# Kernel optimization log

Measured on AMD Instinct MI355X. Metric: run time of the kernel, lower is better.

The kernel has to match this reference:

```python
import jax, jax.numpy as jnp
import numpy as np

NEG_INF = -9.0e15  # matches torch's -9000000000000000.0 mask value
ALPHA = 0.2        # LeakyReLU negative slope


def setup_inputs() -> dict:
    key = jax.random.key(0)
    k1, k2, k3, k4 = jax.random.split(key, 4)
    N, F_in, F_out = 8192, 128, 128
    x = jax.random.normal(k1, (N, F_in), dtype=jnp.float32)
    adj = jax.random.randint(k2, (N, N), 0, 2, dtype=jnp.int32)
    W = jax.random.normal(k3, (F_in, F_out), dtype=jnp.float32) * (1.0 / np.sqrt(F_in))
    a = jax.random.normal(k4, (2 * F_out, 1), dtype=jnp.float32) * (1.0 / np.sqrt(2 * F_out))
    return {"x": x, "adj": adj, "W": W, "a": a}


def reference(x, adj, W, a):
    # h = W(input): [N, F_out]
    h = x @ W
    F_out = h.shape[1]
    # a([h_i || h_j]) = h_i . a[:F] + h_j . a[F:]  -- identical math to the
    # original NxNx2F concat, without materializing it.
    a_src = a[:F_out, 0]   # coefficients on the row (i) node
    a_dst = a[F_out:, 0]   # coefficients on the column (j) node
    s_src = h @ a_src      # [N]
    s_dst = h @ a_dst      # [N]
    e = jax.nn.leaky_relu(s_src[:, None] + s_dst[None, :], negative_slope=ALPHA)  # [N, N]
    e = jnp.where(adj > 0, e, jnp.float32(NEG_INF))
    attention = jax.nn.softmax(e, axis=1)
    # dropout omitted (identity at eval) for a deterministic baseline
    h_prime = attention @ h  # [N, F_out]
    return h_prime
```

## Files before the change

kernel.cpp:

```cpp
#include <hip/hip_runtime.h>

#define N 8192
#define F 128
#define ALPHA 0.2f

typedef __attribute__((ext_vector_type(8))) short short8;
typedef __attribute__((ext_vector_type(4))) float f32x4;
typedef unsigned short u16;

__device__ __forceinline__ u16 f2bf(float f) {
    unsigned int u = __float_as_uint(f);
    u += 0x7fff + ((u >> 16) & 1);
    return (u16)(u >> 16);
}
__device__ __forceinline__ float bf2f(u16 b) {
    return __uint_as_float(((unsigned int)b) << 16);
}
__device__ __forceinline__ float lrelu(float z) { return fmaxf(z, ALPHA * z); }

__global__ __launch_bounds__(256) void gemm_h(const float* __restrict__ x,
                                              const float* __restrict__ W,
                                              const float* __restrict__ aa,
                                              u16* __restrict__ hT,
                                              float* __restrict__ ssrc,
                                              float* __restrict__ sdst) {
    __shared__ float xs[32 * 128];
    __shared__ float Wsh[32 * 128];
    const int t = threadIdx.x;
    const int i0 = blockIdx.x * 32;
    const int c4 = (t & 31) * 4;
    const int r8 = t >> 5;

#pragma unroll
    for (int p = 0; p < 4; ++p) {
        int rr = p * 8 + r8;
        *(float4*)&xs[rr * 128 + c4] = *(const float4*)&x[(size_t)(i0 + rr) * 128 + c4];
    }

    const int tx = t & 31, ty = t >> 5;
    const int r0 = ty * 4, c0 = tx * 4;
    float acc[4][4] = {};

    for (int kc = 0; kc < 4; ++kc) {
        __syncthreads();
#pragma unroll
        for (int p = 0; p < 4; ++p) {
            int k = p * 8 + r8;
            *(float4*)&Wsh[k * 128 + c4] = *(const float4*)&W[(kc * 32 + k) * 128 + c4];
        }
        __syncthreads();
#pragma unroll 4
        for (int k = 0; k < 32; k += 4) {
            float xr[4][4];
#pragma unroll
            for (int rr = 0; rr < 4; ++rr)
                *(float4*)xr[rr] = *(const float4*)&xs[(r0 + rr) * 128 + kc * 32 + k];
#pragma unroll
            for (int kk = 0; kk < 4; ++kk) {
                float4 wv = *(const float4*)&Wsh[(k + kk) * 128 + c0];
#pragma unroll
                for (int rr = 0; rr < 4; ++rr) {
                    acc[rr][0] += xr[rr][kk] * wv.x;
                    acc[rr][1] += xr[rr][kk] * wv.y;
                    acc[rr][2] += xr[rr][kk] * wv.z;
                    acc[rr][3] += xr[rr][kk] * wv.w;
                }
            }
        }
    }

#pragma unroll
    for (int rr = 0; rr < 4; ++rr)
#pragma unroll
        for (int cc = 0; cc < 4; ++cc)
            hT[(size_t)(c0 + cc) * N + (i0 + r0 + rr)] = f2bf(acc[rr][cc]);

    float4 asv = *(const float4*)&aa[c0];
    float4 adv = *(const float4*)&aa[F + c0];
#pragma unroll
    for (int rr = 0; rr < 4; ++rr) {
        float vs = acc[rr][0] * asv.x + acc[rr][1] * asv.y + acc[rr][2] * asv.z + acc[rr][3] * asv.w;
        float vd = acc[rr][0] * adv.x + acc[rr][1] * adv.y + acc[rr][2] * adv.z + acc[rr][3] * adv.w;
#pragma unroll
        for (int off = 16; off >= 1; off >>= 1) {
            vs += __shfl_down(vs, off, 32);
            vd += __shfl_down(vd, off, 32);
        }
        if (tx == 0) {
            ssrc[i0 + r0 + rr] = vs;
            sdst[i0 + r0 + rr] = vd;
        }
    }
}

__global__ __launch_bounds__(256, 2) void attn_mfma(const int* __restrict__ adj,
                                                    const u16* __restrict__ hT,
                                                    const float* __restrict__ ssrc,
                                                    const float* __restrict__ sdst,
                                                    float* __restrict__ out,
                                                    float* __restrict__ pacc1,
                                                    float* __restrict__ pS) {
    __shared__ short8 wsh[2][4][64];
    __shared__ float srow[2][2][16];

    const int t = threadIdx.x;
    const int w = t >> 6, L = t & 63;
    const int quad = L >> 4, l16 = L & 15;
    const int i0 = blockIdx.x * 32;
    const int split = blockIdx.y;
    const int jbase = split * (N / 2);
    const int NC = (N / 2) / 64;

    const int rt = w & 1, ks = w >> 1;
    const int fragid = rt * 2 + ks;
    const int prow = i0 + rt * 16 + l16;
    const float s_i = ssrc[prow];

    const int* pA = adj + (size_t)prow * N + jbase + ks * 32 + quad * 8;
    const float* pD = sdst + jbase + ks * 32 + quad * 8;
    const u16* pB = hT + (size_t)(w * 32 + l16) * N + jbase + quad * 8;

    f32x4 acc[2][2];
#pragma unroll
    for (int a = 0; a < 2; ++a)
#pragma unroll
        for (int b = 0; b < 2; ++b) acc[a][b] = 0.f;
    float rsum = 0.f;

    auto compute_write = [&](int buf, int4 a0, int4 a1, float4 d0, float4 d1) {
        int m[8] = {a0.x, a0.y, a0.z, a0.w, a1.x, a1.y, a1.z, a1.w};
        float d[8] = {d0.x, d0.y, d0.z, d0.w, d1.x, d1.y, d1.z, d1.w};
        short8 pk;
        float s = 0.f;
#pragma unroll
        for (int k = 0; k < 8; ++k) {
            float e = __expf(lrelu(s_i + d[k]));
            float wv = (m[k] > 0) ? e : 0.f;
            u16 b = f2bf(wv);
            s += bf2f(b);
            pk[k] = (short)b;
        }
        rsum += s;
        wsh[buf][fragid][L] = pk;
    };

    int4 aC0 = *(const int4*)(pA);
    int4 aC1 = *(const int4*)(pA + 4);
    float4 dC0 = *(const float4*)(pD);
    float4 dC1 = *(const float4*)(pD + 4);
    compute_write(0, aC0, aC1, dC0, dC1);

    short8 Bbuf[2][2];
#pragma unroll
    for (int c2 = 0; c2 < 2; ++c2)
#pragma unroll
        for (int kb = 0; kb < 2; ++kb)
            Bbuf[c2][kb] = *(const short8*)(pB + (size_t)c2 * 16 * N + kb * 32);

    int4 aN0 = *(const int4*)(pA + 64);
    int4 aN1 = *(const int4*)(pA + 64 + 4);
    float4 dN0 = *(const float4*)(pD + 64);
    float4 dN1 = *(const float4*)(pD + 64 + 4);

    for (int c = 1; c < NC; ++c) {
        __syncthreads();
        const int coff = c * 64;

        short8 Bload[2][2];
#pragma unroll
        for (int c2 = 0; c2 < 2; ++c2)
#pragma unroll
            for (int kb = 0; kb < 2; ++kb)
                Bload[c2][kb] = *(const short8*)(pB + (size_t)c2 * 16 * N + kb * 32 + coff);

        const int cn = (c + 1 < NC) ? c + 1 : NC - 1;
        int4 aP0 = *(const int4*)(pA + cn * 64);
        int4 aP1 = *(const int4*)(pA + cn * 64 + 4);
        float4 dP0 = *(const float4*)(pD + cn * 64);
        float4 dP1 = *(const float4*)(pD + cn * 64 + 4);

        short8 af[4];
#pragma unroll
        for (int fs = 0; fs < 4; ++fs) af[fs] = wsh[(c - 1) & 1][fs][L];
#pragma unroll
        for (int c2 = 0; c2 < 2; ++c2)
#pragma unroll
            for (int rc = 0; rc < 2; ++rc)
#pragma unroll
                for (int kb = 0; kb < 2; ++kb)
                    acc[c2][rc] = __builtin_amdgcn_mfma_f32_16x16x32_bf16(
                        af[rc * 2 + kb], Bbuf[c2][kb], acc[c2][rc], 0, 0, 0);

        compute_write(c & 1, aN0, aN1, dN0, dN1);

        aN0 = aP0; aN1 = aP1; dN0 = dP0; dN1 = dP1;
#pragma unroll
        for (int c2 = 0; c2 < 2; ++c2)
#pragma unroll
            for (int kb = 0; kb < 2; ++kb) Bbuf[c2][kb] = Bload[c2][kb];
    }

    __syncthreads();
    {
        short8 af[4];
#pragma unroll
        for (int fs = 0; fs < 4; ++fs) af[fs] = wsh[(NC - 1) & 1][fs][L];
#pragma unroll
        for (int c2 = 0; c2 < 2; ++c2)
#pragma unroll
            for (int rc = 0; rc < 2; ++rc)
#pragma unroll
                for (int kb = 0; kb < 2; ++kb)
                    acc[c2][rc] = __builtin_amdgcn_mfma_f32_16x16x32_bf16(
                        af[rc * 2 + kb], Bbuf[c2][kb], acc[c2][rc], 0, 0, 0);
    }

    float* dst = split ? pacc1 : out;
#pragma unroll
    for (int c2 = 0; c2 < 2; ++c2) {
        const int col = (w * 2 + c2) * 16 + l16;
#pragma unroll
        for (int rc = 0; rc < 2; ++rc) {
            const int row0 = i0 + rc * 16 + quad * 4;
#pragma unroll
            for (int r = 0; r < 4; ++r)
                dst[(size_t)(row0 + r) * F + col] = acc[c2][rc][r];
        }
    }

    rsum += __shfl_xor(rsum, 16);
    rsum += __shfl_xor(rsum, 32);
    if (L < 16) srow[rt][ks][l16] = rsum;
    __syncthreads();
    if (t < 32) pS[split * N + i0 + t] = srow[t >> 4][0][t & 15] + srow[t >> 4][1][t & 15];
}

__global__ __launch_bounds__(256) void finalize(float* __restrict__ out,
                                                const float* __restrict__ pacc1,
                                                const float* __restrict__ pS) {
    const int idx = (blockIdx.x * 256 + threadIdx.x) * 4;
    const int i = idx >> 7;
    const float inv = 1.0f / (pS[i] + pS[N + i]);
    float4 a0 = *(const float4*)&out[idx];
    float4 a1 = *(const float4*)&pacc1[idx];
    float4 o = {(a0.x + a1.x) * inv, (a0.y + a1.y) * inv,
                (a0.z + a1.z) * inv, (a0.w + a1.w) * inv};
    *(float4*)&out[idx] = o;
}

extern "C" void kernel_launch(void* const* d_in, const int* in_sizes, int n_in,
                              void* d_out, int out_size, void* d_ws, size_t ws_size,
                              hipStream_t stream) {
    (void)in_sizes; (void)n_in; (void)out_size; (void)ws_size;
    const float* x   = (const float*)d_in[0];
    const int*   adj = (const int*)d_in[1];
    const float* W   = (const float*)d_in[2];
    const float* a   = (const float*)d_in[3];
    float* out = (float*)d_out;

    u16* hT     = (u16*)d_ws;
    float* ssrc = (float*)(hT + (size_t)N * F);
    float* sdst = ssrc + N;
    float* pS   = sdst + N;
    float* pacc1 = pS + 2 * N;

    gemm_h<<<N / 32, 256, 0, stream>>>(x, W, a, hT, ssrc, sdst);
    attn_mfma<<<dim3(N / 32, 2), 256, 0, stream>>>(adj, hT, ssrc, sdst, out, pacc1, pS);
    finalize<<<(N * F / 4) / 256, 256, 0, stream>>>(out, pacc1, pS);
}
```

Measured before the change: 413.1 us.

## Split attention columns four ways, deepen adjacency prefetch, use packed bf16 convert

The column range of the attention kernel is split into four parts instead of two. This launches 1024 blocks, raises the occupancy hint to 3 blocks per CU, and makes finalize reduce four partial accumulators and row sums. The adjacency loads are now prefetched two chunks ahead, and the weight computation is moved before the MFMA in each iteration. The manual bf16 rounding is replaced with the v_cvt_pk_bf16_f32 packed-convert instruction. The aim is better latency hiding on the adj stream, which is the main memory traffic, at the cost of more partial-sum traffic in finalize and more register pressure.

```diff
diff --git a/kernel.cpp b/kernel.cpp
--- a/kernel.cpp
+++ b/kernel.cpp
@@ -3,6 +3,7 @@
 #define N 8192
 #define F 128
 #define ALPHA 0.2f
+#define NSPLIT 4
 
 typedef __attribute__((ext_vector_type(8))) short short8;
 typedef __attribute__((ext_vector_type(4))) float f32x4;
@@ -13,10 +14,6 @@
     u += 0x7fff + ((u >> 16) & 1);
     return (u16)(u >> 16);
 }
-__device__ __forceinline__ float bf2f(u16 b) {
-    return __uint_as_float(((unsigned int)b) << 16);
-}
-__device__ __forceinline__ float lrelu(float z) { return fmaxf(z, ALPHA * z); }
 
 __global__ __launch_bounds__(256) void gemm_h(const float* __restrict__ x,
                                               const float* __restrict__ W,
@@ -93,12 +90,12 @@
     }
 }
 
-__global__ __launch_bounds__(256, 2) void attn_mfma(const int* __restrict__ adj,
+__global__ __launch_bounds__(256, 3) void attn_mfma(const int* __restrict__ adj,
                                                     const u16* __restrict__ hT,
                                                     const float* __restrict__ ssrc,
                                                     const float* __restrict__ sdst,
                                                     float* __restrict__ out,
-                                                    float* __restrict__ pacc1,
+                                                    float* __restrict__ pacc,
                                                     float* __restrict__ pS) {
     __shared__ short8 wsh[2][4][64];
     __shared__ float srow[2][2][16];
@@ -108,8 +105,9 @@
     const int quad = L >> 4, l16 = L & 15;
     const int i0 = blockIdx.x * 32;
     const int split = blockIdx.y;
-    const int jbase = split * (N / 2);
-    const int NC = (N / 2) / 64;
+    const int JW = N / NSPLIT;
+    const int jbase = split * JW;
+    const int NC = JW / 64;
 
     const int rt = w & 1, ks = w >> 1;
     const int fragid = rt * 2 + ks;
@@ -128,27 +126,41 @@
     float rsum = 0.f;
 
     auto compute_write = [&](int buf, int4 a0, int4 a1, float4 d0, float4 d1) {
-        int m[8] = {a0.x, a0.y, a0.z, a0.w, a1.x, a1.y, a1.z, a1.w};
-        float d[8] = {d0.x, d0.y, d0.z, d0.w, d1.x, d1.y, d1.z, d1.w};
-        short8 pk;
+        const int m[8] = {a0.x, a0.y, a0.z, a0.w, a1.x, a1.y, a1.z, a1.w};
+        const float d[8] = {d0.x, d0.y, d0.z, d0.w, d1.x, d1.y, d1.z, d1.w};
+        float wv[8];
+#pragma unroll
+        for (int k = 0; k < 8; ++k) {
+            float z = s_i + d[k];
+            float e = __expf(fmaxf(z, ALPHA * z));
+            wv[k] = (m[k] > 0) ? e : 0.f;
+        }
+        union { unsigned int u[4]; short8 s8; } pk;
         float s = 0.f;
 #pragma unroll
-        for (int k = 0; k < 8; ++k) {
-            float e = __expf(lrelu(s_i + d[k]));
-            float wv = (m[k] > 0) ? e : 0.f;
-            u16 b = f2bf(wv);
-            s += bf2f(b);
-            pk[k] = (short)b;
+        for (int p = 0; p < 4; ++p) {
+            unsigned int r;
+            asm("v_cvt_pk_bf16_f32 %0, %1, %2" : "=v"(r) : "v"(wv[2 * p]), "v"(wv[2 * p + 1]));
+            pk.u[p] = r;
+            s += __uint_as_float(r << 16);
+            s += __uint_as_float(r & 0xffff0000u);
         }
         rsum += s;
-        wsh[buf][fragid][L] = pk;
+        wsh[buf][fragid][L] = pk.s8;
     };
 
-    int4 aC0 = *(const int4*)(pA);
-    int4 aC1 = *(const int4*)(pA + 4);
-    float4 dC0 = *(const float4*)(pD);
-    float4 dC1 = *(const float4*)(pD + 4);
-    compute_write(0, aC0, aC1, dC0, dC1);
+    int4 aN0 = *(const int4*)(pA);
+    int4 aN1 = *(const int4*)(pA + 4);
+    int4 aP0 = *(const int4*)(pA + 64);
+    int4 aP1 = *(const int4*)(pA + 68);
+    float4 dN0 = *(const float4*)(pD);
+    float4 dN1 = *(const float4*)(pD + 4);
+    compute_write(0, aN0, aN1, dN0, dN1);
+    aN0 = aP0; aN1 = aP1;
+    aP0 = *(const int4*)(pA + 128);
+    aP1 = *(const int4*)(pA + 132);
+    dN0 = *(const float4*)(pD + 64);
+    dN1 = *(const float4*)(pD + 68);
 
     short8 Bbuf[2][2];
 #pragma unroll
@@ -156,11 +168,6 @@
 #pragma unroll
         for (int kb = 0; kb < 2; ++kb)
             Bbuf[c2][kb] = *(const short8*)(pB + (size_t)c2 * 16 * N + kb * 32);
-
-    int4 aN0 = *(const int4*)(pA + 64);
-    int4 aN1 = *(const int4*)(pA + 64 + 4);
-    float4 dN0 = *(const float4*)(pD + 64);
-    float4 dN1 = *(const float4*)(pD + 64 + 4);
 
     for (int c = 1; c < NC; ++c) {
         __syncthreads();
@@ -173,11 +180,15 @@
             for (int kb = 0; kb < 2; ++kb)
                 Bload[c2][kb] = *(const short8*)(pB + (size_t)c2 * 16 * N + kb * 32 + coff);
 
-        const int cn = (c + 1 < NC) ? c + 1 : NC - 1;
-        int4 aP0 = *(const int4*)(pA + cn * 64);
-        int4 aP1 = *(const int4*)(pA + cn * 64 + 4);
-        float4 dP0 = *(const float4*)(pD + cn * 64);
-        float4 dP1 = *(const float4*)(pD + cn * 64 + 4);
+        compute_write(c & 1, aN0, aN1, dN0, dN1);
+
+        aN0 = aP0; aN1 = aP1;
+        const int ca = (c + 2 < NC) ? c + 2 : NC - 1;
+        aP0 = *(const int4*)(pA + ca * 64);
+        aP1 = *(const int4*)(pA + ca * 64 + 4);
+        const int cd = (c + 1 < NC) ? c + 1 : NC - 1;
+        dN0 = *(const float4*)(pD + cd * 64);
+        dN1 = *(const float4*)(pD + cd * 64 + 4);
 
         short8 af[4];
 #pragma unroll
@@ -191,9 +202,6 @@
                     acc[c2][rc] = __builtin_amdgcn_mfma_f32_16x16x32_bf16(
                         af[rc * 2 + kb], Bbuf[c2][kb], acc[c2][rc], 0, 0, 0);
 
-        compute_write(c & 1, aN0, aN1, dN0, dN1);
-
-        aN0 = aP0; aN1 = aP1; dN0 = dP0; dN1 = dP1;
 #pragma unroll
         for (int c2 = 0; c2 < 2; ++c2)
 #pragma unroll
@@ -215,7 +223,7 @@
                         af[rc * 2 + kb], Bbuf[c2][kb], acc[c2][rc], 0, 0, 0);
     }
 
-    float* dst = split ? pacc1 : out;
+    float* dst = split ? pacc + (size_t)(split - 1) * N * F : out;
 #pragma unroll
     for (int c2 = 0; c2 < 2; ++c2) {
         const int col = (w * 2 + c2) * 16 + l16;
@@ -236,15 +244,19 @@
 }
 
 __global__ __launch_bounds__(256) void finalize(float* __restrict__ out,
-                                                const float* __restrict__ pacc1,
+                                                const float* __restrict__ pacc,
                                                 const float* __restrict__ pS) {
     const int idx = (blockIdx.x * 256 + threadIdx.x) * 4;
     const int i = idx >> 7;
-    const float inv = 1.0f / (pS[i] + pS[N + i]);
+    const float inv = 1.0f / (pS[i] + pS[N + i] + pS[2 * N + i] + pS[3 * N + i]);
     float4 a0 = *(const float4*)&out[idx];
-    float4 a1 = *(const float4*)&pacc1[idx];
-    float4 o = {(a0.x + a1.x) * inv, (a0.y + a1.y) * inv,
-                (a0.z + a1.z) * inv, (a0.w + a1.w) * inv};
+    float4 a1 = *(const float4*)&pacc[idx];
+    float4 a2 = *(const float4*)&pacc[(size_t)N * F + idx];
+    float4 a3 = *(const float4*)&pacc[2 * (size_t)N * F + idx];
+    float4 o = {(a0.x + a1.x + a2.x + a3.x) * inv,
+                (a0.y + a1.y + a2.y + a3.y) * inv,
+                (a0.z + a1.z + a2.z + a3.z) * inv,
+                (a0.w + a1.w + a2.w + a3.w) * inv};
     *(float4*)&out[idx] = o;
 }
 
@@ -262,9 +274,9 @@
     float* ssrc = (float*)(hT + (size_t)N * F);
     float* sdst = ssrc + N;
     float* pS   = sdst + N;
-    float* pacc1 = pS + 2 * N;
+    float* pacc = pS + NSPLIT * N;
 
     gemm_h<<<N / 32, 256, 0, stream>>>(x, W, a, hT, ssrc, sdst);
-    attn_mfma<<<dim3(N / 32, 2), 256, 0, stream>>>(adj, hT, ssrc, sdst, out, pacc1, pS);
-    finalize<<<(N * F / 4) / 256, 256, 0, stream>>>(out, pacc1, pS);
-}
+    attn_mfma<<<dim3(N / 32, NSPLIT), 256, 0, stream>>>(adj, hT, ssrc, sdst, out, pacc, pS);
+    finalize<<<(N * F / 4) / 256, 256, 0, stream>>>(out, pacc, pS);
+}
```

After: 417.5 us. No clear change (+1.1%).
